# Kernel tuning notes

Hardware: AMD Instinct MI355X
Metric: run time of the kernel (lower is better)

Reference implementation:

```python
import jax, jax.numpy as jnp
import numpy as np

EPS = 1e-6

def rms_norm(x):
    return x * jax.lax.rsqrt(jnp.mean(x * x, axis=-1, keepdims=True) + EPS)

def setup_inputs() -> dict:
    key = jax.random.key(0)
    k_x, k_w = jax.random.split(key)
    T, B, D = 2048, 16, 1024
    x = jax.random.normal(k_x, (T, B, D), dtype=jnp.float32)
    h0 = jnp.zeros((B, D), dtype=jnp.float32)
    # xavier_uniform for W: limit = sqrt(6/(fan_in+fan_out)) = sqrt(6/(2D))
    limit = float(np.sqrt(6.0 / (2 * D)))
    W = jax.random.uniform(k_w, (D, D), dtype=jnp.float32, minval=-limit, maxval=limit)
    b = jnp.zeros((D,), dtype=jnp.float32)
    log_alpha = jnp.asarray(np.log(0.1), dtype=jnp.float32)
    return {"x": x, "h0": h0, "W": W, "b": b, "log_alpha": log_alpha}

def reference(x, h0, W, b, log_alpha):
    # x: [T,B,D], h0: [B,D], W: [D,D], b: [D], log_alpha: []
    alpha = jnp.exp(log_alpha)
    # Precompute all input projections in one big GEMM: [T,B,D]
    Wx_all = jnp.einsum('tbd,ed->tbe', x, W) + b

    def step(h, wx):
        h_new = rms_norm(h + alpha * wx)
        out = h_new * jax.nn.silu(h_new)
        return h_new, (h_new, out)

    _, (hs, outs) = jax.lax.scan(step, h0, Wx_all)
    h = jnp.concatenate([h0[None], hs], axis=0)  # [T+1,B,D]
    return outs, h
```

## Files before the change

kernel.cpp:

```cpp
#include <hip/hip_runtime.h>
#include <hip/hip_bf16.h>

#define T_STEPS 2048
#define BATCH 16
#define DIM 1024
#define EPSV 1e-6f

typedef short short8 __attribute__((ext_vector_type(8)));
typedef float f32x4 __attribute__((ext_vector_type(4)));

struct alignas(16) bf16x8pack { __hip_bfloat16 v[8]; };

__global__ __launch_bounds__(256) void cvt_kernel(const float* __restrict__ src,
                                                  bf16x8pack* __restrict__ dst, int n8) {
  int i = blockIdx.x * blockDim.x + threadIdx.x;
  if (i >= n8) return;
  const float4* s4 = (const float4*)src + (size_t)i * 2;
  float4 a = s4[0];
  float4 b = s4[1];
  bf16x8pack p;
  p.v[0] = __float2bfloat16(a.x); p.v[1] = __float2bfloat16(a.y);
  p.v[2] = __float2bfloat16(a.z); p.v[3] = __float2bfloat16(a.w);
  p.v[4] = __float2bfloat16(b.x); p.v[5] = __float2bfloat16(b.y);
  p.v[6] = __float2bfloat16(b.z); p.v[7] = __float2bfloat16(b.w);
  dst[i] = p;
}

__global__ __launch_bounds__(256) void gemm_kernel(
    const __hip_bfloat16* __restrict__ Xb,
    const __hip_bfloat16* __restrict__ Wb,
    const float* __restrict__ bias,
    const float* __restrict__ log_alpha_p,
    float* __restrict__ hreg) {
  __shared__ __hip_bfloat16 As[128 * 32];
  __shared__ __hip_bfloat16 Bs[128 * 32];
  const int tid = threadIdx.x;
  const int wave = tid >> 6, lane = tid & 63;
  const int m0 = blockIdx.y * 128;
  const int e0 = blockIdx.x * 128;
  const int wm = (wave >> 1) * 64;
  const int wn = (wave & 1) * 64;
  const int l15 = lane & 15, l4 = lane >> 4;

  f32x4 acc[4][4] = {};

  const int srow = wave * 16 + (lane >> 2);
  const int sch = (lane & 3) * 8;

  for (int kt = 0; kt < DIM; kt += 32) {
    __syncthreads();
#pragma unroll
    for (int i = 0; i < 2; ++i) {
      const __hip_bfloat16* ga = Xb + (size_t)(m0 + i * 64 + srow) * DIM + kt + sch;
      const __hip_bfloat16* gb = Wb + (size_t)(e0 + i * 64 + srow) * DIM + kt + sch;
      __builtin_amdgcn_global_load_lds(
          (const __attribute__((address_space(1))) void*)ga,
          (__attribute__((address_space(3))) void*)((char*)As + (i * 64 + wave * 16) * 64),
          16, 0, 0);
      __builtin_amdgcn_global_load_lds(
          (const __attribute__((address_space(1))) void*)gb,
          (__attribute__((address_space(3))) void*)((char*)Bs + (i * 64 + wave * 16) * 64),
          16, 0, 0);
    }
    __syncthreads();
    short8 a[4], b[4];
#pragma unroll
    for (int f = 0; f < 4; ++f)
      a[f] = *(const short8*)((const char*)As + ((wm + f * 16 + l15) * 32 + l4 * 8) * 2);
#pragma unroll
    for (int g = 0; g < 4; ++g)
      b[g] = *(const short8*)((const char*)Bs + ((wn + g * 16 + l15) * 32 + l4 * 8) * 2);
#pragma unroll
    for (int f = 0; f < 4; ++f)
#pragma unroll
      for (int g = 0; g < 4; ++g)
        acc[f][g] = __builtin_amdgcn_mfma_f32_16x16x32_bf16(a[f], b[g], acc[f][g], 0, 0, 0);
  }
  const float alpha = __expf(log_alpha_p[0]);
#pragma unroll
  for (int g = 0; g < 4; ++g) {
    const int e = e0 + wn + g * 16 + l15;
    const float bv = bias[e];
#pragma unroll
    for (int f = 0; f < 4; ++f) {
#pragma unroll
      for (int r = 0; r < 4; ++r) {
        const int m = m0 + wm + f * 16 + l4 * 4 + r;
        hreg[(size_t)(m + BATCH) * DIM + e] = alpha * (acc[f][g][r] + bv);
      }
    }
  }
}

__device__ __forceinline__ float wave_sum_dpp(float x) {
  float acc = x;
#define DPP_ADD(ctrl)                                                              \
  {                                                                                \
    int t_ = __builtin_amdgcn_update_dpp(0, __float_as_int(acc), (ctrl), 0xf, 0xf, \
                                         true);                                    \
    acc += __int_as_float(t_);                                                     \
  }
  DPP_ADD(0x111);
  DPP_ADD(0x112);
  DPP_ADD(0x114);
  DPP_ADD(0x118);
  DPP_ADD(0x142);
  DPP_ADD(0x143);
#undef DPP_ADD
  return __int_as_float(__builtin_amdgcn_readlane(__float_as_int(acc), 63));
}

__global__ __launch_bounds__(64) void scan_kernel(
    const float* __restrict__ h0,
    float* __restrict__ hreg) {
  const int b = blockIdx.x;
  const int lane = threadIdx.x;
  const float4* h04 = (const float4*)h0;
  float4* h4 = (float4*)hreg;
  const int base = b * 256 + lane;
  const size_t SLOT4 = (size_t)BATCH * DIM / 4;

  float4 s[4], wx[4][4];
#pragma unroll
  for (int j = 0; j < 4; ++j) s[j] = h04[base + 64 * j];
#pragma unroll
  for (int j = 0; j < 4; ++j) h4[base + 64 * j] = s[j];
#pragma unroll
  for (int p = 0; p < 4; ++p)
#pragma unroll
    for (int j = 0; j < 4; ++j) wx[p][j] = h4[SLOT4 * (size_t)(p + 1) + base + 64 * j];

  float rinv = 1.0f;

#pragma unroll 4
  for (int t = 0; t < T_STEPS; ++t) {
    const int ph = t & 3;
    float4 sn[4];
    float p0 = 0.f, p1 = 0.f, p2 = 0.f, p3 = 0.f;
#pragma unroll
    for (int j = 0; j < 4; ++j) {
      sn[j].x = fmaf(rinv, s[j].x, wx[ph][j].x);
      sn[j].y = fmaf(rinv, s[j].y, wx[ph][j].y);
      sn[j].z = fmaf(rinv, s[j].z, wx[ph][j].z);
      sn[j].w = fmaf(rinv, s[j].w, wx[ph][j].w);
      p0 = fmaf(sn[j].x, sn[j].x, p0);
      p1 = fmaf(sn[j].y, sn[j].y, p1);
      p2 = fmaf(sn[j].z, sn[j].z, p2);
      p3 = fmaf(sn[j].w, sn[j].w, p3);
    }
    float sum = wave_sum_dpp((p0 + p1) + (p2 + p3));
    {
      float4 hv[4];
#pragma unroll
      for (int j = 0; j < 4; ++j) {
        hv[j].x = s[j].x * rinv; hv[j].y = s[j].y * rinv;
        hv[j].z = s[j].z * rinv; hv[j].w = s[j].w * rinv;
      }
      if (t > 0) {
#pragma unroll
        for (int j = 0; j < 4; ++j) h4[SLOT4 * (size_t)t + base + 64 * j] = hv[j];
      }
    }
    if (t + 4 < T_STEPS) {
#pragma unroll
      for (int j = 0; j < 4; ++j) wx[ph][j] = h4[SLOT4 * (size_t)(t + 5) + base + 64 * j];
    }
    rinv = rsqrtf(fmaf(sum, 1.0f / DIM, EPSV));
#pragma unroll
    for (int j = 0; j < 4; ++j) s[j] = sn[j];
  }
#pragma unroll
  for (int j = 0; j < 4; ++j) {
    float4 hv;
    hv.x = s[j].x * rinv; hv.y = s[j].y * rinv;
    hv.z = s[j].z * rinv; hv.w = s[j].w * rinv;
    h4[SLOT4 * (size_t)T_STEPS + base + 64 * j] = hv;
  }
}

__global__ __launch_bounds__(256) void silu_kernel(const float4* __restrict__ hsrc,
                                                   float4* __restrict__ out4, int n4) {
  int i = blockIdx.x * blockDim.x + threadIdx.x;
  if (i >= n4) return;
  float4 h = hsrc[i];
  float4 o;
  o.x = h.x * h.x / (1.f + __expf(-h.x));
  o.y = h.y * h.y / (1.f + __expf(-h.y));
  o.z = h.z * h.z / (1.f + __expf(-h.z));
  o.w = h.w * h.w / (1.f + __expf(-h.w));
  out4[i] = o;
}

extern "C" void kernel_launch(void* const* d_in, const int* in_sizes, int n_in,
                              void* d_out, int out_size, void* d_ws, size_t ws_size,
                              hipStream_t stream) {
  (void)in_sizes; (void)n_in; (void)d_ws; (void)ws_size; (void)out_size;
  const float* x = (const float*)d_in[0];
  const float* h0 = (const float*)d_in[1];
  const float* W = (const float*)d_in[2];
  const float* bias = (const float*)d_in[3];
  const float* log_alpha = (const float*)d_in[4];

  float* out = (float*)d_out;
  float* hreg = out + (size_t)T_STEPS * BATCH * DIM;
  __hip_bfloat16* xb = (__hip_bfloat16*)d_out;
  __hip_bfloat16* wb = (__hip_bfloat16*)((char*)d_out + (size_t)T_STEPS * BATCH * DIM * 2);

  const int nx8 = T_STEPS * BATCH * DIM / 8;
  const int nw8 = DIM * DIM / 8;
  cvt_kernel<<<nx8 / 256, 256, 0, stream>>>(x, (bf16x8pack*)xb, nx8);
  cvt_kernel<<<nw8 / 256, 256, 0, stream>>>(W, (bf16x8pack*)wb, nw8);

  dim3 ggrid(DIM / 128, (T_STEPS * BATCH) / 128);
  gemm_kernel<<<ggrid, 256, 0, stream>>>(xb, wb, bias, log_alpha, hreg);

  scan_kernel<<<BATCH, 64, 0, stream>>>(h0, hreg);

  const int n4 = T_STEPS * BATCH * DIM / 4;
  silu_kernel<<<n4 / 256, 256, 0, stream>>>((const float4*)(hreg + BATCH * DIM),
                                            (float4*)out, n4);
}
```

Measured before the change: 583.5 us.

## Precompute wx dot products so the scan reduction is off the critical path

A new parallel kernel precomputes, for every step, |wx_t|^2 and the dot products of wx_t with wx_{t-1} and wx_{t-2}. The scan then updates the squared norm algebraically from these scalars and a lagged reduction of h·wx, which is started two steps ahead. This takes the per-step wave reduction out of the serial dependency chain and overlaps it with later steps. In exchange it adds an extra pass over the whole hreg buffer, more registers, and possible numerical drift from the incremental norm recurrence. It also uses an ad hoc scratch region inside the output buffer.

```diff
diff --git a/kernel.cpp b/kernel.cpp
--- a/kernel.cpp
+++ b/kernel.cpp
@@ -5,6 +5,8 @@
 #define BATCH 16
 #define DIM 1024
 #define EPSV 1e-6f
+#define SLOTF (BATCH * DIM)
+#define SLOT4C (BATCH * DIM / 4)
 
 typedef short short8 __attribute__((ext_vector_type(8)));
 typedef float f32x4 __attribute__((ext_vector_type(4)));
@@ -92,7 +94,7 @@
   }
 }
 
-__device__ __forceinline__ float wave_sum_dpp(float x) {
+__device__ __forceinline__ float dpp_sum_reg(float x) {
   float acc = x;
 #define DPP_ADD(ctrl)                                                              \
   {                                                                                \
@@ -100,81 +102,158 @@
                                          true);                                    \
     acc += __int_as_float(t_);                                                     \
   }
-  DPP_ADD(0x111);
-  DPP_ADD(0x112);
-  DPP_ADD(0x114);
-  DPP_ADD(0x118);
-  DPP_ADD(0x142);
-  DPP_ADD(0x143);
+  DPP_ADD(0x111); DPP_ADD(0x112); DPP_ADD(0x114); DPP_ADD(0x118);
+  DPP_ADD(0x142); DPP_ADD(0x143);
 #undef DPP_ADD
-  return __int_as_float(__builtin_amdgcn_readlane(__float_as_int(acc), 63));
+  return acc;
+}
+__device__ __forceinline__ float lane63(float v) {
+  return __int_as_float(__builtin_amdgcn_readlane(__float_as_int(v), 63));
+}
+
+__global__ __launch_bounds__(64) void dots_kernel(const float* __restrict__ hreg,
+                                                  float4* __restrict__ scal4) {
+  const int t = blockIdx.x >> 4;
+  const int b = blockIdx.x & 15;
+  const int lane = threadIdx.x;
+  const float4* w  = (const float4*)(hreg + (size_t)(t + 1) * SLOTF + b * DIM);
+  const float4* m1 = (const float4*)(hreg + (size_t)(t    ) * SLOTF + b * DIM);
+  const float4* m2 = (const float4*)(hreg + (size_t)(t - 1) * SLOTF + b * DIM);
+  float e = 0.f, d = 0.f, d2 = 0.f;
+#pragma unroll
+  for (int j = 0; j < 4; ++j) {
+    float4 a = w[lane + 64 * j];
+    e = fmaf(a.x, a.x, fmaf(a.y, a.y, fmaf(a.z, a.z, fmaf(a.w, a.w, e))));
+    if (t >= 1) {
+      float4 p = m1[lane + 64 * j];
+      d = fmaf(p.x, a.x, fmaf(p.y, a.y, fmaf(p.z, a.z, fmaf(p.w, a.w, d))));
+    }
+    if (t >= 2) {
+      float4 p = m2[lane + 64 * j];
+      d2 = fmaf(p.x, a.x, fmaf(p.y, a.y, fmaf(p.z, a.z, fmaf(p.w, a.w, d2))));
+    }
+  }
+  e = dpp_sum_reg(e);
+  d = dpp_sum_reg(d);
+  d2 = dpp_sum_reg(d2);
+  if (lane == 63) scal4[b * T_STEPS + t] = make_float4(e, d, d2, 0.f);
 }
 
 __global__ __launch_bounds__(64) void scan_kernel(
     const float* __restrict__ h0,
+    const float4* __restrict__ scal4,
     float* __restrict__ hreg) {
   const int b = blockIdx.x;
   const int lane = threadIdx.x;
-  const float4* h04 = (const float4*)h0;
   float4* h4 = (float4*)hreg;
   const int base = b * 256 + lane;
-  const size_t SLOT4 = (size_t)BATCH * DIM / 4;
-
-  float4 s[4], wx[4][4];
-#pragma unroll
-  for (int j = 0; j < 4; ++j) s[j] = h04[base + 64 * j];
+  const float4* sc_base = scal4 + b * T_STEPS;
+
+  float4 s[4], hv[4], wx[6][4], sc[6];
+  float greg[2];
+
+  float4 w0[4], w1[4];
+#pragma unroll
+  for (int j = 0; j < 4; ++j) w0[j] = h4[(size_t)SLOT4C * 1 + base + 64 * j];
+#pragma unroll
+  for (int j = 0; j < 4; ++j) w1[j] = h4[(size_t)SLOT4C * 2 + base + 64 * j];
+#pragma unroll
+  for (int p = 0; p < 6; ++p) {
+#pragma unroll
+    for (int j = 0; j < 4; ++j)
+      wx[(2 + p) % 6][j] = h4[(size_t)SLOT4C * (3 + p) + base + 64 * j];
+    sc[(2 + p) % 6] = sc_base[2 + p];
+  }
+  const float e1 = sc_base[1].x;
+
+#pragma unroll
+  for (int j = 0; j < 4; ++j) s[j] = ((const float4*)h0)[base + 64 * j];
 #pragma unroll
   for (int j = 0; j < 4; ++j) h4[base + 64 * j] = s[j];
-#pragma unroll
-  for (int p = 0; p < 4; ++p)
-#pragma unroll
-    for (int j = 0; j < 4; ++j) wx[p][j] = h4[SLOT4 * (size_t)(p + 1) + base + 64 * j];
-
-  float rinv = 1.0f;
-
-#pragma unroll 4
-  for (int t = 0; t < T_STEPS; ++t) {
-    const int ph = t & 3;
-    float4 sn[4];
-    float p0 = 0.f, p1 = 0.f, p2 = 0.f, p3 = 0.f;
-#pragma unroll
-    for (int j = 0; j < 4; ++j) {
-      sn[j].x = fmaf(rinv, s[j].x, wx[ph][j].x);
-      sn[j].y = fmaf(rinv, s[j].y, wx[ph][j].y);
-      sn[j].z = fmaf(rinv, s[j].z, wx[ph][j].z);
-      sn[j].w = fmaf(rinv, s[j].w, wx[ph][j].w);
-      p0 = fmaf(sn[j].x, sn[j].x, p0);
-      p1 = fmaf(sn[j].y, sn[j].y, p1);
-      p2 = fmaf(sn[j].z, sn[j].z, p2);
-      p3 = fmaf(sn[j].w, sn[j].w, p3);
-    }
-    float sum = wave_sum_dpp((p0 + p1) + (p2 + p3));
-    {
-      float4 hv[4];
+  float4 s1[4];
+  float q0 = 0, q1 = 0, q2 = 0, q3 = 0;
+  float r0 = 0, r1 = 0, r2 = 0, r3 = 0;
+  float u0 = 0, u1 = 0, u2 = 0, u3 = 0;
+#pragma unroll
+  for (int j = 0; j < 4; ++j) {
+    s1[j].x = s[j].x + w0[j].x; s1[j].y = s[j].y + w0[j].y;
+    s1[j].z = s[j].z + w0[j].z; s1[j].w = s[j].w + w0[j].w;
+    q0 = fmaf(s1[j].x, s1[j].x, q0); q1 = fmaf(s1[j].y, s1[j].y, q1);
+    q2 = fmaf(s1[j].z, s1[j].z, q2); q3 = fmaf(s1[j].w, s1[j].w, q3);
+    r0 = fmaf(s1[j].x, w1[j].x, r0); r1 = fmaf(s1[j].y, w1[j].y, r1);
+    r2 = fmaf(s1[j].z, w1[j].z, r2); r3 = fmaf(s1[j].w, w1[j].w, r3);
+    u0 = fmaf(s[j].x, wx[2][j].x, u0); u1 = fmaf(s[j].y, wx[2][j].y, u1);
+    u2 = fmaf(s[j].z, wx[2][j].z, u2); u3 = fmaf(s[j].w, wx[2][j].w, u3);
+  }
+  const float n1 = lane63(dpp_sum_reg((q0 + q1) + (q2 + q3)));
+  const float b1 = lane63(dpp_sum_reg((r0 + r1) + (r2 + r3)));
+  greg[0] = dpp_sum_reg((u0 + u1) + (u2 + u3));
+
+  float rinv = rsqrtf(fmaf(n1, 1.0f / DIM, EPSV));
+  float v0 = 0, v1 = 0, v2 = 0, v3 = 0;
+#pragma unroll
+  for (int j = 0; j < 4; ++j) {
+    hv[j].x = rinv * s1[j].x; hv[j].y = rinv * s1[j].y;
+    hv[j].z = rinv * s1[j].z; hv[j].w = rinv * s1[j].w;
+  }
+#pragma unroll
+  for (int j = 0; j < 4; ++j) h4[(size_t)SLOT4C * 1 + base + 64 * j] = hv[j];
+#pragma unroll
+  for (int j = 0; j < 4; ++j) {
+    s[j].x = hv[j].x + w1[j].x; s[j].y = hv[j].y + w1[j].y;
+    s[j].z = hv[j].z + w1[j].z; s[j].w = hv[j].w + w1[j].w;
+    v0 = fmaf(hv[j].x, wx[3][j].x, v0); v1 = fmaf(hv[j].y, wx[3][j].y, v1);
+    v2 = fmaf(hv[j].z, wx[3][j].z, v2); v3 = fmaf(hv[j].w, wx[3][j].w, v3);
+  }
+  float n = fmaf(rinv, fmaf(rinv, n1, 2.0f * b1), e1);
+  greg[1] = dpp_sum_reg((v0 + v1) + (v2 + v3));
+  float rinv_im1 = rinv;
+
+  for (int ii = 2; ii < T_STEPS; ii += 6) {
+#pragma unroll
+    for (int k = 0; k < 6; ++k) {
+      const int i = ii + k;
+      const int s0i = (2 + k) % 6;
+      const int s2i = (4 + k) % 6;
+      const int par = k & 1;
+      const float rinv_i = rsqrtf(fmaf(n, 1.0f / DIM, EPSV));
+      const float g = lane63(greg[par]);
+      const float bb = fmaf(rinv_im1, g + sc[s0i].z, sc[s0i].y);
+      n = fmaf(rinv_i, fmaf(rinv_i, n, 2.0f * bb), sc[s0i].x);
+      float p0 = 0, p1 = 0, p2 = 0, p3 = 0;
 #pragma unroll
       for (int j = 0; j < 4; ++j) {
-        hv[j].x = s[j].x * rinv; hv[j].y = s[j].y * rinv;
-        hv[j].z = s[j].z * rinv; hv[j].w = s[j].w * rinv;
+        hv[j].x = rinv_i * s[j].x; hv[j].y = rinv_i * s[j].y;
+        hv[j].z = rinv_i * s[j].z; hv[j].w = rinv_i * s[j].w;
       }
-      if (t > 0) {
-#pragma unroll
-        for (int j = 0; j < 4; ++j) h4[SLOT4 * (size_t)t + base + 64 * j] = hv[j];
+#pragma unroll
+      for (int j = 0; j < 4; ++j)
+        h4[(size_t)SLOT4C * i + base + 64 * j] = hv[j];
+#pragma unroll
+      for (int j = 0; j < 4; ++j) {
+        s[j].x = hv[j].x + wx[s0i][j].x; s[j].y = hv[j].y + wx[s0i][j].y;
+        s[j].z = hv[j].z + wx[s0i][j].z; s[j].w = hv[j].w + wx[s0i][j].w;
+        p0 = fmaf(hv[j].x, wx[s2i][j].x, p0);
+        p1 = fmaf(hv[j].y, wx[s2i][j].y, p1);
+        p2 = fmaf(hv[j].z, wx[s2i][j].z, p2);
+        p3 = fmaf(hv[j].w, wx[s2i][j].w, p3);
       }
-    }
-    if (t + 4 < T_STEPS) {
-#pragma unroll
-      for (int j = 0; j < 4; ++j) wx[ph][j] = h4[SLOT4 * (size_t)(t + 5) + base + 64 * j];
-    }
-    rinv = rsqrtf(fmaf(sum, 1.0f / DIM, EPSV));
-#pragma unroll
-    for (int j = 0; j < 4; ++j) s[j] = sn[j];
-  }
-#pragma unroll
-  for (int j = 0; j < 4; ++j) {
-    float4 hv;
-    hv.x = s[j].x * rinv; hv.y = s[j].y * rinv;
-    hv.z = s[j].z * rinv; hv.w = s[j].w * rinv;
-    h4[SLOT4 * (size_t)T_STEPS + base + 64 * j] = hv;
+      greg[par] = dpp_sum_reg((p0 + p1) + (p2 + p3));
+      const int ipf = (i + 6 < T_STEPS) ? (i + 6) : (T_STEPS - 1);
+#pragma unroll
+      for (int j = 0; j < 4; ++j)
+        wx[s0i][j] = h4[(size_t)SLOT4C * (ipf + 1) + base + 64 * j];
+      sc[s0i] = sc_base[ipf];
+      rinv_im1 = rinv_i;
+    }
+  }
+  const float rinv_T = rsqrtf(fmaf(n, 1.0f / DIM, EPSV));
+#pragma unroll
+  for (int j = 0; j < 4; ++j) {
+    float4 o;
+    o.x = rinv_T * s[j].x; o.y = rinv_T * s[j].y;
+    o.z = rinv_T * s[j].z; o.w = rinv_T * s[j].w;
+    h4[(size_t)SLOT4C * T_STEPS + base + 64 * j] = o;
   }
 }
 
@@ -205,6 +284,7 @@
   float* hreg = out + (size_t)T_STEPS * BATCH * DIM;
   __hip_bfloat16* xb = (__hip_bfloat16*)d_out;
   __hip_bfloat16* wb = (__hip_bfloat16*)((char*)d_out + (size_t)T_STEPS * BATCH * DIM * 2);
+  float4* scal4 = (float4*)(out + (size_t)26 * 1024 * 1024);
 
   const int nx8 = T_STEPS * BATCH * DIM / 8;
   const int nw8 = DIM * DIM / 8;
@@ -214,7 +294,9 @@
   dim3 ggrid(DIM / 128, (T_STEPS * BATCH) / 128);
   gemm_kernel<<<ggrid, 256, 0, stream>>>(xb, wb, bias, log_alpha, hreg);
 
-  scan_kernel<<<BATCH, 64, 0, stream>>>(h0, hreg);
+  dots_kernel<<<T_STEPS * BATCH, 64, 0, stream>>>(hreg, scal4);
+
+  scan_kernel<<<BATCH, 64, 0, stream>>>(h0, scal4, hreg);
 
   const int n4 = T_STEPS * BATCH * DIM / 4;
   silu_kernel<<<n4 / 256, 256, 0, stream>>>((const float4*)(hreg + BATCH * DIM),
```

Result: slower. 744.3 us (+27.6%).

## Precompute lagged dot products and split scan across four waves per batch

Applied to the files above, without the earlier changes.

Adds a parallel dots_kernel that precomputes the squared norms of the projected inputs and their dot products with the previous three steps. The scan kernel uses these to update the running squared norm algebraically, so each step only needs one cross-wave partial sum delayed by a few steps. That lets the scan run with 256 threads per batch row instead of one wave, shortening the serial per-step work. The cost is an extra kernel pass over the whole activation tensor, a workgroup barrier every step, and more rounding error from the expanded norm recurrence.

```diff
diff --git a/kernel.cpp b/kernel.cpp
--- a/kernel.cpp
+++ b/kernel.cpp
@@ -5,6 +5,9 @@
 #define BATCH 16
 #define DIM 1024
 #define EPSV 1e-6f
+#define INVD (1.0f / 1024.0f)
+#define SLOTF (BATCH * DIM)
+#define SLOT4C (BATCH * DIM / 4)
 
 typedef short short8 __attribute__((ext_vector_type(8)));
 typedef float f32x4 __attribute__((ext_vector_type(4)));
@@ -92,7 +95,7 @@
   }
 }
 
-__device__ __forceinline__ float wave_sum_dpp(float x) {
+__device__ __forceinline__ float dpp_sum_reg(float x) {
   float acc = x;
 #define DPP_ADD(ctrl)                                                              \
   {                                                                                \
@@ -100,82 +103,173 @@
                                          true);                                    \
     acc += __int_as_float(t_);                                                     \
   }
-  DPP_ADD(0x111);
-  DPP_ADD(0x112);
-  DPP_ADD(0x114);
-  DPP_ADD(0x118);
-  DPP_ADD(0x142);
-  DPP_ADD(0x143);
+  DPP_ADD(0x111); DPP_ADD(0x112); DPP_ADD(0x114); DPP_ADD(0x118);
+  DPP_ADD(0x142); DPP_ADD(0x143);
 #undef DPP_ADD
-  return __int_as_float(__builtin_amdgcn_readlane(__float_as_int(acc), 63));
-}
-
-__global__ __launch_bounds__(64) void scan_kernel(
+  return acc;
+}
+
+__global__ __launch_bounds__(64) void dots_kernel(const float* __restrict__ hreg,
+                                                  float4* __restrict__ scal4) {
+  const int t = blockIdx.x >> 4;
+  const int b = blockIdx.x & 15;
+  const int lane = threadIdx.x;
+  const float4* w  = (const float4*)(hreg + (size_t)(t + 1) * SLOTF + b * DIM);
+  const float4* m1 = (const float4*)(hreg + (size_t)(t    ) * SLOTF + b * DIM);
+  const float4* m2 = (const float4*)(hreg + (size_t)(t - 1) * SLOTF + b * DIM);
+  const float4* m3 = (const float4*)(hreg + (size_t)(t - 2) * SLOTF + b * DIM);
+  float e = 0.f, d = 0.f, d2 = 0.f, d3 = 0.f;
+#pragma unroll
+  for (int j = 0; j < 4; ++j) {
+    float4 a = w[lane + 64 * j];
+    e = fmaf(a.x, a.x, fmaf(a.y, a.y, fmaf(a.z, a.z, fmaf(a.w, a.w, e))));
+    if (t >= 1) {
+      float4 p = m1[lane + 64 * j];
+      d = fmaf(p.x, a.x, fmaf(p.y, a.y, fmaf(p.z, a.z, fmaf(p.w, a.w, d))));
+    }
+    if (t >= 2) {
+      float4 p = m2[lane + 64 * j];
+      d2 = fmaf(p.x, a.x, fmaf(p.y, a.y, fmaf(p.z, a.z, fmaf(p.w, a.w, d2))));
+    }
+    if (t >= 3) {
+      float4 p = m3[lane + 64 * j];
+      d3 = fmaf(p.x, a.x, fmaf(p.y, a.y, fmaf(p.z, a.z, fmaf(p.w, a.w, d3))));
+    }
+  }
+  e = dpp_sum_reg(e);
+  d = dpp_sum_reg(d);
+  d2 = dpp_sum_reg(d2);
+  d3 = dpp_sum_reg(d3);
+  if (lane == 63) scal4[b * T_STEPS + t] = make_float4(e, d, d2, d3);
+}
+
+__global__ __launch_bounds__(256) void scan_kernel(
     const float* __restrict__ h0,
+    const float4* __restrict__ scal4,
     float* __restrict__ hreg) {
   const int b = blockIdx.x;
-  const int lane = threadIdx.x;
-  const float4* h04 = (const float4*)h0;
+  const int tid = threadIdx.x;
+  const int wave = tid >> 6;
+  const int lane = tid & 63;
   float4* h4 = (float4*)hreg;
-  const int base = b * 256 + lane;
-  const size_t SLOT4 = (size_t)BATCH * DIM / 4;
-
-  float4 s[4], wx[4][4];
-#pragma unroll
-  for (int j = 0; j < 4; ++j) s[j] = h04[base + 64 * j];
-#pragma unroll
-  for (int j = 0; j < 4; ++j) h4[base + 64 * j] = s[j];
-#pragma unroll
-  for (int p = 0; p < 4; ++p)
-#pragma unroll
-    for (int j = 0; j < 4; ++j) wx[p][j] = h4[SLOT4 * (size_t)(p + 1) + base + 64 * j];
-
-  float rinv = 1.0f;
-
-#pragma unroll 4
-  for (int t = 0; t < T_STEPS; ++t) {
-    const int ph = t & 3;
-    float4 sn[4];
-    float p0 = 0.f, p1 = 0.f, p2 = 0.f, p3 = 0.f;
-#pragma unroll
-    for (int j = 0; j < 4; ++j) {
-      sn[j].x = fmaf(rinv, s[j].x, wx[ph][j].x);
-      sn[j].y = fmaf(rinv, s[j].y, wx[ph][j].y);
-      sn[j].z = fmaf(rinv, s[j].z, wx[ph][j].z);
-      sn[j].w = fmaf(rinv, s[j].w, wx[ph][j].w);
-      p0 = fmaf(sn[j].x, sn[j].x, p0);
-      p1 = fmaf(sn[j].y, sn[j].y, p1);
-      p2 = fmaf(sn[j].z, sn[j].z, p2);
-      p3 = fmaf(sn[j].w, sn[j].w, p3);
-    }
-    float sum = wave_sum_dpp((p0 + p1) + (p2 + p3));
-    {
-      float4 hv[4];
-#pragma unroll
-      for (int j = 0; j < 4; ++j) {
-        hv[j].x = s[j].x * rinv; hv[j].y = s[j].y * rinv;
-        hv[j].z = s[j].z * rinv; hv[j].w = s[j].w * rinv;
-      }
-      if (t > 0) {
-#pragma unroll
-        for (int j = 0; j < 4; ++j) h4[SLOT4 * (size_t)t + base + 64 * j] = hv[j];
-      }
-    }
-    if (t + 4 < T_STEPS) {
-#pragma unroll
-      for (int j = 0; j < 4; ++j) wx[ph][j] = h4[SLOT4 * (size_t)(t + 5) + base + 64 * j];
-    }
-    rinv = rsqrtf(fmaf(sum, 1.0f / DIM, EPSV));
-#pragma unroll
-    for (int j = 0; j < 4; ++j) s[j] = sn[j];
-  }
-#pragma unroll
-  for (int j = 0; j < 4; ++j) {
+  const int idx4 = b * 256 + tid;
+
+  __shared__ float4 scLDS[T_STEPS];
+  __shared__ float Gp[4][4];
+  __shared__ float initP[4][8];
+
+#pragma unroll
+  for (int p = 0; p < 8; ++p)
+    scLDS[p * 256 + tid] = scal4[b * T_STEPS + p * 256 + tid];
+
+  float4 w[8];
+  w[2] = h4[(size_t)SLOT4C * 3 + idx4];
+  w[3] = h4[(size_t)SLOT4C * 4 + idx4];
+  w[4] = h4[(size_t)SLOT4C * 5 + idx4];
+  w[5] = h4[(size_t)SLOT4C * 6 + idx4];
+  w[6] = h4[(size_t)SLOT4C * 7 + idx4];
+  w[7] = h4[(size_t)SLOT4C * 8 + idx4];
+  w[0] = h4[(size_t)SLOT4C * 9 + idx4];
+  w[1] = h4[(size_t)SLOT4C * 10 + idx4];
+  float4 w0v = h4[(size_t)SLOT4C * 1 + idx4];
+  float4 w1v = h4[(size_t)SLOT4C * 2 + idx4];
+  float4 h0v = ((const float4*)h0)[idx4];
+  h4[idx4] = h0v;
+
+  float4 s;
+  s.x = h0v.x + w0v.x; s.y = h0v.y + w0v.y;
+  s.z = h0v.z + w0v.z; s.w = h0v.w + w0v.w;
+  float q  = fmaf(s.x, s.x, fmaf(s.y, s.y, fmaf(s.z, s.z, s.w * s.w)));
+  float r  = fmaf(s.x, w1v.x, fmaf(s.y, w1v.y, fmaf(s.z, w1v.z, s.w * w1v.w)));
+  float u2 = fmaf(s.x, w[2].x, fmaf(s.y, w[2].y, fmaf(s.z, w[2].z, s.w * w[2].w)));
+  float g3 = fmaf(h0v.x, w[3].x, fmaf(h0v.y, w[3].y, fmaf(h0v.z, w[3].z, h0v.w * w[3].w)));
+  float u4 = fmaf(s.x, w[4].x, fmaf(s.y, w[4].y, fmaf(s.z, w[4].z, s.w * w[4].w)));
+  q = dpp_sum_reg(q); r = dpp_sum_reg(r); u2 = dpp_sum_reg(u2);
+  g3 = dpp_sum_reg(g3); u4 = dpp_sum_reg(u4);
+  if (lane == 63) {
+    initP[wave][0] = q; initP[wave][1] = r; initP[wave][2] = u2;
+    initP[wave][3] = g3; initP[wave][4] = u4;
+  }
+  __syncthreads();
+  const float n1  = initP[0][0] + initP[1][0] + initP[2][0] + initP[3][0];
+  const float b1  = initP[0][1] + initP[1][1] + initP[2][1] + initP[3][1];
+  const float c2  = initP[0][2] + initP[1][2] + initP[2][2] + initP[3][2];
+  const float G3v = initP[0][3] + initP[1][3] + initP[2][3] + initP[3][3];
+  const float c4  = initP[0][4] + initP[1][4] + initP[2][4] + initP[3][4];
+
+  float4 sc0 = scLDS[2];
+  float4 sc1 = scLDS[3];
+  const float e1 = scLDS[1].x;
+
+  const float rinv1 = rsqrtf(fmaf(n1, INVD, EPSV));
+  float n = fmaf(rinv1, fmaf(rinv1, n1, 2.0f * b1), e1);
+  const float b2p = fmaf(rinv1, c2, sc0.y);
+  float gr1 = G3v;
+  float gr0 = rinv1 * c4;
+
+  {
     float4 hv;
-    hv.x = s[j].x * rinv; hv.y = s[j].y * rinv;
-    hv.z = s[j].z * rinv; hv.w = s[j].w * rinv;
-    h4[SLOT4 * (size_t)T_STEPS + base + 64 * j] = hv;
-  }
+    hv.x = rinv1 * s.x; hv.y = rinv1 * s.y; hv.z = rinv1 * s.z; hv.w = rinv1 * s.w;
+    h4[(size_t)SLOT4C * 1 + idx4] = hv;
+    s.x = hv.x + w1v.x; s.y = hv.y + w1v.y; s.z = hv.z + w1v.z; s.w = hv.w + w1v.w;
+  }
+  float rm1 = rinv1, rm2 = 0.0f;
+
+#define STEP(IEXPR, WS, W3S, SCA, GPW, GPR, GRW, GRU, MODE)                          \
+  {                                                                                  \
+    const int i_ = (IEXPR);                                                          \
+    const float rinv = rsqrtf(fmaf(n, INVD, EPSV));                                  \
+    float bb;                                                                        \
+    if ((MODE) == 1) bb = b2p;                                                       \
+    else bb = fmaf(rm1, fmaf(rm2, SCA.w + GRU, SCA.z), SCA.y);                       \
+    n = fmaf(rinv, fmaf(rinv, n, 2.0f * bb), SCA.x);                                 \
+    float4 hv_;                                                                      \
+    hv_.x = rinv * s.x; hv_.y = rinv * s.y;                                          \
+    hv_.z = rinv * s.z; hv_.w = rinv * s.w;                                          \
+    h4[(size_t)SLOT4C * i_ + idx4] = hv_;                                            \
+    s.x = hv_.x + w[WS].x; s.y = hv_.y + w[WS].y;                                    \
+    s.z = hv_.z + w[WS].z; s.w = hv_.w + w[WS].w;                                    \
+    float p_ = fmaf(hv_.x, w[W3S].x, fmaf(hv_.y, w[W3S].y,                           \
+               fmaf(hv_.z, w[W3S].z, hv_.w * w[W3S].w)));                            \
+    p_ = dpp_sum_reg(p_);                                                            \
+    if (lane == 63) Gp[GPW][wave] = p_;                                              \
+    if ((MODE) == 0) {                                                               \
+      float4 g4_ = *(const float4*)&Gp[GPR][0];                                      \
+      GRW = (g4_.x + g4_.y) + (g4_.z + g4_.w);                                       \
+    }                                                                                \
+    const int ipf_ = (i_ + 8 < T_STEPS) ? i_ + 8 : T_STEPS - 1;                      \
+    w[WS] = h4[(size_t)SLOT4C * (ipf_ + 1) + idx4];                                  \
+    const int isc_ = (i_ + 2 < T_STEPS) ? i_ + 2 : T_STEPS - 1;                      \
+    SCA = scLDS[isc_];                                                               \
+    rm2 = rm1; rm1 = rinv;                                                           \
+    asm volatile("s_waitcnt lgkmcnt(0)" ::: "memory");                               \
+    __builtin_amdgcn_sched_barrier(0);                                               \
+    __builtin_amdgcn_s_barrier();                                                    \
+  }
+
+  STEP(2, 2, 5, sc0, 2, 0, gr0, gr1, 1)
+  STEP(3, 3, 6, sc1, 3, 0, gr0, gr1, 2)
+  STEP(4, 4, 7, sc0, 0, 2, gr1, gr0, 0)
+
+  for (int ii = 5; ii <= 2037; ii += 8) {
+    STEP(ii + 0, 5, 0, sc1, 1, 3, gr0, gr1, 0)
+    STEP(ii + 1, 6, 1, sc0, 2, 0, gr1, gr0, 0)
+    STEP(ii + 2, 7, 2, sc1, 3, 1, gr0, gr1, 0)
+    STEP(ii + 3, 0, 3, sc0, 0, 2, gr1, gr0, 0)
+    STEP(ii + 4, 1, 4, sc1, 1, 3, gr0, gr1, 0)
+    STEP(ii + 5, 2, 5, sc0, 2, 0, gr1, gr0, 0)
+    STEP(ii + 6, 3, 6, sc1, 3, 1, gr0, gr1, 0)
+    STEP(ii + 7, 4, 7, sc0, 0, 2, gr1, gr0, 0)
+  }
+  STEP(2045, 5, 0, sc1, 1, 3, gr0, gr1, 0)
+  STEP(2046, 6, 1, sc0, 2, 0, gr1, gr0, 0)
+  STEP(2047, 7, 2, sc1, 3, 1, gr0, gr1, 0)
+#undef STEP
+
+  const float rinvT = rsqrtf(fmaf(n, INVD, EPSV));
+  float4 o;
+  o.x = rinvT * s.x; o.y = rinvT * s.y; o.z = rinvT * s.z; o.w = rinvT * s.w;
+  h4[(size_t)SLOT4C * T_STEPS + idx4] = o;
 }
 
 __global__ __launch_bounds__(256) void silu_kernel(const float4* __restrict__ hsrc,
@@ -205,6 +299,7 @@
   float* hreg = out + (size_t)T_STEPS * BATCH * DIM;
   __hip_bfloat16* xb = (__hip_bfloat16*)d_out;
   __hip_bfloat16* wb = (__hip_bfloat16*)((char*)d_out + (size_t)T_STEPS * BATCH * DIM * 2);
+  float4* scal4 = (float4*)(out + (size_t)26 * 1024 * 1024);
 
   const int nx8 = T_STEPS * BATCH * DIM / 8;
   const int nw8 = DIM * DIM / 8;
@@ -214,7 +309,9 @@
   dim3 ggrid(DIM / 128, (T_STEPS * BATCH) / 128);
   gemm_kernel<<<ggrid, 256, 0, stream>>>(xb, wb, bias, log_alpha, hreg);
 
-  scan_kernel<<<BATCH, 64, 0, stream>>>(h0, hreg);
+  dots_kernel<<<T_STEPS * BATCH, 64, 0, stream>>>(hreg, scal4);
+
+  scan_kernel<<<BATCH, 256, 0, stream>>>(h0, scal4, hreg);
 
   const int n4 = T_STEPS * BATCH * DIM / 4;
   silu_kernel<<<n4 / 256, 256, 0, stream>>>((const float4*)(hreg + BATCH * DIM),
```

After: 609.3 us. 4.4% more time.
